# Kernel optimization log

Hardware: AMD Instinct MI355X
Metric: run time of the kernel (lower is better)

Reference implementation:

```python
import jax, jax.numpy as jnp
import numpy as np

N, E, D, NHID, NOUT, G = 100000, 600000, 128, 512, 768, 2048
EPS = 1e-5

def _lin_init(k, fi, fo):
    s = 1.0 / np.sqrt(fi)
    kw, kb = jax.random.split(k)
    W = jax.random.uniform(kw, (fi, fo), jnp.float32, -s, s)
    b = jax.random.uniform(kb, (fo,), jnp.float32, -s, s)
    return W, b

def setup_inputs():
    key = jax.random.key(0)
    ks = jax.random.split(key, 16)
    inp = {}
    inp['x'] = jax.random.normal(ks[0], (N, D), jnp.float32)
    inp['edge_index'] = jax.random.randint(ks[1], (2, E), 0, N, jnp.int32)
    inp['batch'] = jnp.sort(jax.random.randint(ks[2], (N,), 0, G, jnp.int32))
    # 3 GCN layers + GAT attention layer + 4 MLP linears
    inp['W1'], inp['b1'] = _lin_init(ks[3], D, D)
    inp['W2'], inp['b2'] = _lin_init(ks[4], D, D)
    inp['W3'], inp['b3'] = _lin_init(ks[5], D, D)
    inp['Wa'], inp['ba'] = _lin_init(ks[6], D, D)
    ka1, ka2 = jax.random.split(ks[7])
    inp['a_src'] = jax.random.normal(ka1, (D,), jnp.float32) * 0.1
    inp['a_dst'] = jax.random.normal(ka2, (D,), jnp.float32) * 0.1
    # batchnorm affine params (4 BNs)
    for i, nm in enumerate(['g1', 'g2', 'g3', 'ga']):
        inp[nm] = jnp.ones((D,), jnp.float32)
        inp['be' + nm[1:]] = jnp.zeros((D,), jnp.float32)
    inp['Wl1'], inp['bl1'] = _lin_init(ks[8], D, NHID)
    inp['Wl2'], inp['bl2'] = _lin_init(ks[9], NHID, NHID)
    inp['Wl3'], inp['bl3'] = _lin_init(ks[10], NHID, NHID)
    inp['Wl4'], inp['bl4'] = _lin_init(ks[11], NHID, NOUT)
    inp['gln'] = jnp.ones((NOUT,), jnp.float32)
    inp['bln'] = jnp.zeros((NOUT,), jnp.float32)
    return inp

def _bn(x, g, b):
    # training-mode batchnorm over node dim (biased variance, like torch)
    mu = jnp.mean(x, axis=0)
    var = jnp.var(x, axis=0)
    return (x - mu) * jax.lax.rsqrt(var + EPS) * g + b

def _forward(x, edge_index, batch, W1, b1, g1, be1, W2, b2, g2, be2, W3, b3, g3, be3,
             Wa, ba, a_src, a_dst, ga, bea, Wl1, bl1, Wl2, bl2, Wl3, bl3, Wl4, bl4, gln, bln):
    loop = jnp.arange(N, dtype=edge_index.dtype)
    src = jnp.concatenate([edge_index[0], loop])  # [E+N] with self-loops
    dst = jnp.concatenate([edge_index[1], loop])
    deg = jax.ops.segment_sum(jnp.ones_like(dst, jnp.float32), dst, num_segments=N)
    dinv = jax.lax.rsqrt(deg)  # deg >= 1 thanks to self-loops
    norm = (dinv[src] * dinv[dst])[:, None]  # [E+N, 1]

    def gcn(h, W, b):
        h = h @ W
        return jax.ops.segment_sum(h[src] * norm, dst, num_segments=N) + b

    x = jax.nn.relu(_bn(gcn(x, W1, b1), g1, be1)) + x
    x = jax.nn.relu(_bn(gcn(x, W2, b2), g2, be2)) + x
    x = jax.nn.relu(_bn(gcn(x, W3, b3), g3, be3)) + x

    # GATConv, heads=1: edge logit = LeakyReLU(a_src.h_j + a_dst.h_i), softmax over dst
    h = x @ Wa
    al = h @ a_src  # [N]
    ar = h @ a_dst
    e = jax.nn.leaky_relu(al[src] + ar[dst], 0.2)  # [E+N]
    m = jax.ops.segment_max(e, dst, num_segments=N)
    ee = jnp.exp(e - m[dst])
    denom = jax.ops.segment_sum(ee, dst, num_segments=N)
    alpha = (ee / denom[dst])[:, None]
    x = jax.ops.segment_sum(alpha * h[src], dst, num_segments=N) + ba
    x = jax.nn.relu(_bn(x, ga, bea))

    # global_add_pool
    x = jax.ops.segment_sum(x, batch, num_segments=G)  # [G, D]

    x = jax.nn.relu(x @ Wl1 + bl1)
    x = jax.nn.relu(x @ Wl2 + bl2)
    x = jax.nn.relu(x @ Wl3 + bl3)
    x = x @ Wl4 + bl4
    mu = jnp.mean(x, axis=-1, keepdims=True)
    var = jnp.var(x, axis=-1, keepdims=True)
    return (x - mu) * jax.lax.rsqrt(var + EPS) * gln + bln

def reference(x, edge_index, batch, W1, b1, g1, be1, W2, b2, g2, be2, W3, b3, g3, be3,
              Wa, ba, a_src, a_dst, ga, bea, Wl1, bl1, Wl2, bl2, Wl3, bl3, Wl4, bl4, gln, bln):
    return _forward(x, edge_index, batch, W1, b1, g1, be1, W2, b2, g2, be2, W3, b3, g3, be3,
                    Wa, ba, a_src, a_dst, ga, bea, Wl1, bl1, Wl2, bl2, Wl3, bl3, Wl4, bl4, gln, bln)
```

## Files before the change

kernel.cpp:

```cpp
#include <hip/hip_runtime.h>
#include <cstdint>
#include <cstddef>

#define CDIV(a,b) (((a)+(b)-1)/(b))

constexpr int N_ = 100000;
constexpr int E_ = 600000;
constexpr int D_ = 128;
constexpr int G_ = 2048;
constexpr int NHID_ = 512;
constexpr int NOUT_ = 768;
constexpr float EPS_ = 1e-5f;
constexpr int AGG_BLOCKS = 2048;

typedef short bf16x8 __attribute__((ext_vector_type(8)));
typedef float f32x4 __attribute__((ext_vector_type(4)));

__device__ __forceinline__ float wave_sum(float v){
#pragma unroll
  for (int m = 32; m; m >>= 1) v += __shfl_xor(v, m, 64);
  return v;
}
__device__ __forceinline__ float lrelu02(float v){ return v > 0.f ? v : 0.2f * v; }
__device__ __forceinline__ unsigned short f2bf(float f){
  unsigned u = __float_as_uint(f);
  u += 0x7FFF + ((u >> 16) & 1);
  return (unsigned short)(u >> 16);
}
__device__ __forceinline__ float bflo(unsigned u){ return __uint_as_float(u << 16); }
__device__ __forceinline__ float bfhi(unsigned u){ return __uint_as_float(u & 0xFFFF0000u); }

__device__ __forceinline__ float4 unplo(uint4 u){ return make_float4(bflo(u.x), bflo(u.y), bflo(u.z), bflo(u.w)); }
__device__ __forceinline__ float4 unphi(uint4 u){ return make_float4(bfhi(u.x), bfhi(u.y), bfhi(u.z), bfhi(u.w)); }
__device__ __forceinline__ float4 bnrelu4(float4 v, float4 sc, float4 sh){
  return make_float4(fmaxf(v.x*sc.x+sh.x, 0.f), fmaxf(v.y*sc.y+sh.y, 0.f),
                     fmaxf(v.z*sc.z+sh.z, 0.f), fmaxf(v.w*sc.w+sh.w, 0.f));
}
__device__ __forceinline__ float4 add4(float4 a, float4 b){
  return make_float4(a.x+b.x, a.y+b.y, a.z+b.z, a.w+b.w);
}
__device__ __forceinline__ uint4 pk4(float4 lo, float4 hi){
  uint4 u;
  u.x = (unsigned)f2bf(lo.x) | ((unsigned)f2bf(hi.x) << 16);
  u.y = (unsigned)f2bf(lo.y) | ((unsigned)f2bf(hi.y) << 16);
  u.z = (unsigned)f2bf(lo.z) | ((unsigned)f2bf(hi.z) << 16);
  u.w = (unsigned)f2bf(lo.w) | ((unsigned)f2bf(hi.w) << 16);
  return u;
}
__device__ __forceinline__ bf16x8 mkaf(float4 lo, float4 hi){
  bf16x8 a;
  a[0]=(short)f2bf(lo.x); a[1]=(short)f2bf(lo.y); a[2]=(short)f2bf(lo.z); a[3]=(short)f2bf(lo.w);
  a[4]=(short)f2bf(hi.x); a[5]=(short)f2bf(hi.y); a[6]=(short)f2bf(hi.z); a[7]=(short)f2bf(hi.w);
  return a;
}

__global__ void k_count(const int* __restrict__ dst, int* __restrict__ cnt){
  int e = blockIdx.x * 256 + threadIdx.x;
  if (e < E_) atomicAdd(&cnt[dst[e]], 1);
}

__global__ void k_dinv(const int* __restrict__ cnt, float* __restrict__ dinv){
  int i = blockIdx.x * 256 + threadIdx.x;
  if (i < N_) dinv[i] = rsqrtf((float)(cnt[i] + 1));
}

__global__ void k_scan1(const int* __restrict__ cnt, int* __restrict__ ro, int* __restrict__ bs){
  __shared__ int s[256];
  int tid = threadIdx.x;
  int i = blockIdx.x * 256 + tid;
  int v = (i < N_) ? cnt[i] : 0;
  s[tid] = v; __syncthreads();
  for (int off = 1; off < 256; off <<= 1){
    int add = (tid >= off) ? s[tid - off] : 0;
    __syncthreads();
    s[tid] += add;
    __syncthreads();
  }
  if (i < N_) ro[i] = s[tid] - v;
  if (tid == 255) bs[blockIdx.x] = s[255];
}

__global__ void k_scan2(int* __restrict__ bs, int nb){
  __shared__ int s[512];
  int t = threadIdx.x;
  int v = (t < nb) ? bs[t] : 0;
  s[t] = v; __syncthreads();
  for (int off = 1; off < 512; off <<= 1){
    int a = (t >= off) ? s[t - off] : 0;
    __syncthreads();
    s[t] += a;
    __syncthreads();
  }
  if (t < nb) bs[t] = s[t] - v;
}

__global__ void k_scan3(int* __restrict__ ro, const int* __restrict__ bs){
  int i = blockIdx.x * 256 + threadIdx.x;
  if (i < N_) ro[i] += bs[i >> 8];
  if (i == N_) ro[N_] = E_;
}

__global__ void k_fill(const int* __restrict__ src, const int* __restrict__ dst,
                       const int* __restrict__ ro, int* __restrict__ cur, int* __restrict__ csr){
  int e = blockIdx.x * 256 + threadIdx.x;
  if (e < E_){
    int d = dst[e];
    int p = atomicAdd(&cur[d], 1);
    csr[ro[d] + p] = src[e];
  }
}

__global__ void k_bounds(const int* __restrict__ batch, int* __restrict__ gs){
  int g = blockIdx.x * 256 + threadIdx.x;
  if (g > G_) return;
  int lo = 0, hi = N_;
  while (lo < hi){ int mid = (lo + hi) >> 1; if (batch[mid] < g) lo = mid + 1; else hi = mid; }
  gs[g] = lo;
}

__global__ void k_wprep(const float* __restrict__ W, short* __restrict__ Wt){
  int i = blockIdx.x * 256 + threadIdx.x;
  if (i >= 128 * 16) return;
  int c = i >> 4, tg = i & 15, t = tg >> 2, g = tg & 3;
  short* o = Wt + (size_t)i * 8;
#pragma unroll
  for (int j = 0; j < 8; ++j){
    int k = t * 32 + (j >> 2) * 16 + g * 4 + (j & 3);
    o[j] = (short)f2bf(W[(size_t)k * 128 + c]);
  }
}

template<bool XB, bool RB>
__global__ __launch_bounds__(256) void k_mm_mfma(const void* __restrict__ Xin,
                                                 const short* __restrict__ Wt,
                                                 unsigned* __restrict__ hout,
                                                 const float* __restrict__ ss,
                                                 const void* __restrict__ resin,
                                                 unsigned* __restrict__ xnew,
                                                 const float* __restrict__ prescale,
                                                 const float* __restrict__ asrc,
                                                 const float* __restrict__ adst,
                                                 float* __restrict__ al_out,
                                                 float* __restrict__ ar_out){
  int lane = threadIdx.x & 63, wid = threadIdx.x >> 6;
  int cl = lane & 15, g = lane >> 4;
  int r0a = blockIdx.x * 128 + wid * 16;
  int r0b = r0a + 64;
  int rowa = r0a + cl, rowb = r0b + cl;
  bool va_ = rowa < N_, vb_ = rowb < N_;
  int rma = va_ ? rowa : 0;
  int rmb = vb_ ? rowb : 0;

  uint4 xua[4], xub[4];
  float4 xfa[8], xfb[8];
  uint4 rua[4], rub[4];
  float4 rfa[8], rfb[8];
  bool has_res = resin != nullptr;
  if (XB){
    const uint4* Xa = (const uint4*)((const unsigned*)Xin + (size_t)rma * 64);
    const uint4* Xb = (const uint4*)((const unsigned*)Xin + (size_t)rmb * 64);
#pragma unroll
    for (int t = 0; t < 4; ++t){ xua[t] = Xa[t*4 + g]; xub[t] = Xb[t*4 + g]; }
  } else {
    const float4* Xa = (const float4*)((const float*)Xin + (size_t)rma * 128);
    const float4* Xb = (const float4*)((const float*)Xin + (size_t)rmb * 128);
#pragma unroll
    for (int t = 0; t < 4; ++t){
      xfa[2*t] = Xa[t*8 + g]; xfa[2*t+1] = Xa[t*8 + g + 4];
      xfb[2*t] = Xb[t*8 + g]; xfb[2*t+1] = Xb[t*8 + g + 4];
    }
  }
  if (has_res){
    if (RB){
      const uint4* Ra = (const uint4*)((const unsigned*)resin + (size_t)rma * 64);
      const uint4* Rb = (const uint4*)((const unsigned*)resin + (size_t)rmb * 64);
#pragma unroll
      for (int t = 0; t < 4; ++t){ rua[t] = Ra[t*4 + g]; rub[t] = Rb[t*4 + g]; }
    } else {
      const float4* Ra = (const float4*)((const float*)resin + (size_t)rma * 128);
      const float4* Rb = (const float4*)((const float*)resin + (size_t)rmb * 128);
#pragma unroll
      for (int t = 0; t < 4; ++t){
        rfa[2*t] = Ra[t*8 + g]; rfa[2*t+1] = Ra[t*8 + g + 4];
        rfb[2*t] = Rb[t*8 + g]; rfb[2*t+1] = Rb[t*8 + g + 4];
      }
    }
  }
  __builtin_amdgcn_sched_barrier(0);

  bf16x8 afa[4], afb[4];
#pragma unroll
  for (int t = 0; t < 4; ++t){
    float4 la, ha, lb, hb;
    if (XB){
      la = unplo(xua[t]); ha = unphi(xua[t]);
      lb = unplo(xub[t]); hb = unphi(xub[t]);
    } else {
      la = xfa[2*t]; ha = xfa[2*t+1];
      lb = xfb[2*t]; hb = xfb[2*t+1];
    }
    if (ss){
      int f0 = t * 32 + g * 4;
      float4 sc0 = *(const float4*)&ss[f0],      sh0 = *(const float4*)&ss[128 + f0];
      float4 sc1 = *(const float4*)&ss[f0 + 16], sh1 = *(const float4*)&ss[128 + f0 + 16];
      la = bnrelu4(la, sc0, sh0); ha = bnrelu4(ha, sc1, sh1);
      lb = bnrelu4(lb, sc0, sh0); hb = bnrelu4(hb, sc1, sh1);
      if (has_res){
        if (RB){
          la = add4(la, unplo(rua[t])); ha = add4(ha, unphi(rua[t]));
          lb = add4(lb, unplo(rub[t])); hb = add4(hb, unphi(rub[t]));
        } else {
          la = add4(la, rfa[2*t]); ha = add4(ha, rfa[2*t+1]);
          lb = add4(lb, rfb[2*t]); hb = add4(hb, rfb[2*t+1]);
        }
      }
      if (xnew){
        if (va_) *(uint4*)(xnew + (size_t)rowa * 64 + t*16 + g*4) = pk4(la, ha);
        if (vb_) *(uint4*)(xnew + (size_t)rowb * 64 + t*16 + g*4) = pk4(lb, hb);
      }
    }
    afa[t] = mkaf(la, ha);
    afb[t] = mkaf(lb, hb);
  }

  f32x4 accA[8], accB[8];
#pragma unroll
  for (int j = 0; j < 8; ++j){ accA[j] = (f32x4){0,0,0,0}; accB[j] = (f32x4){0,0,0,0}; }
#pragma unroll
  for (int t = 0; t < 4; ++t){
#pragma unroll
    for (int j = 0; j < 8; ++j){
      int c = j * 16 + cl;
      bf16x8 bf = *(const bf16x8*)(Wt + ((size_t)c * 16 + t * 4 + g) * 8);
      accA[j] = __builtin_amdgcn_mfma_f32_16x16x32_bf16(afa[t], bf, accA[j], 0, 0, 0);
      accB[j] = __builtin_amdgcn_mfma_f32_16x16x32_bf16(afb[t], bf, accB[j], 0, 0, 0);
    }
  }

#pragma unroll
  for (int r = 0; r < 4; ++r){
    int ra = r0a + g * 4 + r;
    if (ra < N_){
      float psc = prescale ? prescale[ra] : 1.f;
#pragma unroll
      for (int jp = 0; jp < 4; ++jp){
        unsigned lo = f2bf(accA[2*jp][r] * psc);
        unsigned hi = f2bf(accA[2*jp+1][r] * psc);
        hout[(size_t)ra * 64 + jp * 16 + cl] = (hi << 16) | lo;
      }
    }
    int rb = r0b + g * 4 + r;
    if (rb < N_){
      float psc = prescale ? prescale[rb] : 1.f;
#pragma unroll
      for (int jp = 0; jp < 4; ++jp){
        unsigned lo = f2bf(accB[2*jp][r] * psc);
        unsigned hi = f2bf(accB[2*jp+1][r] * psc);
        hout[(size_t)rb * 64 + jp * 16 + cl] = (hi << 16) | lo;
      }
    }
  }

  if (al_out){
    float pal[8] = {0,0,0,0,0,0,0,0}, par[8] = {0,0,0,0,0,0,0,0};
#pragma unroll
    for (int j = 0; j < 8; ++j){
      float as_ = asrc[j * 16 + cl], ad_ = adst[j * 16 + cl];
#pragma unroll
      for (int r = 0; r < 4; ++r){
        pal[r]   += accA[j][r] * as_; par[r]   += accA[j][r] * ad_;
        pal[4+r] += accB[j][r] * as_; par[4+r] += accB[j][r] * ad_;
      }
    }
#pragma unroll
    for (int m = 1; m < 16; m <<= 1)
#pragma unroll
      for (int r = 0; r < 8; ++r){
        pal[r] += __shfl_xor(pal[r], m, 64);
        par[r] += __shfl_xor(par[r], m, 64);
      }
    if (cl == 0){
#pragma unroll
      for (int r = 0; r < 4; ++r){
        int ra = r0a + g * 4 + r;
        if (ra < N_){ al_out[ra] = pal[r]; ar_out[ra] = par[r]; }
        int rb = r0b + g * 4 + r;
        if (rb < N_){ al_out[rb] = pal[4+r]; ar_out[rb] = par[4+r]; }
      }
    }
  }
}

__global__ __launch_bounds__(256) void k_gcn_agg2(const unsigned* __restrict__ hbf, const int* __restrict__ ro,
                          const int* __restrict__ csr, const float* __restrict__ dinv,
                          const float* __restrict__ bias, unsigned* __restrict__ outb,
                          float4* __restrict__ pbuf){
  int wid = threadIdx.x >> 6, lane = threadIdx.x & 63;
  int f0 = 32 * (lane >> 4) + (lane & 15), f1 = f0 + 16;
  float bb0 = bias[f0], bb1 = bias[f1];
  float S0 = 0.f, S1 = 0.f, Q0 = 0.f, Q1 = 0.f;
  for (int node = blockIdx.x * 4 + wid; node < N_; node += AGG_BLOCKS * 4){
    int s0 = ro[node], s1 = ro[node + 1];
    int deg = s1 - s0;
    float di = dinv[node];
    unsigned us = hbf[(size_t)node * 64 + lane];
    float a0 = bflo(us), a1 = bfhi(us);
    if (deg <= 64){
      int sidx = (lane < deg) ? csr[s0 + lane] : 0;
      int j = 0;
      for (; j + 4 <= deg; j += 4){
        int sa = __shfl(sidx, j, 64),   sb = __shfl(sidx, j+1, 64);
        int sc = __shfl(sidx, j+2, 64), sd = __shfl(sidx, j+3, 64);
        unsigned ua = hbf[(size_t)sa*64+lane], ub = hbf[(size_t)sb*64+lane];
        unsigned uc = hbf[(size_t)sc*64+lane], ud = hbf[(size_t)sd*64+lane];
        a0 += bflo(ua) + bflo(ub) + bflo(uc) + bflo(ud);
        a1 += bfhi(ua) + bfhi(ub) + bfhi(uc) + bfhi(ud);
      }
      for (; j < deg; ++j){
        int s = __shfl(sidx, j, 64);
        unsigned u = hbf[(size_t)s*64+lane];
        a0 += bflo(u); a1 += bfhi(u);
      }
    } else {
      for (int base = s0; base < s1; base += 64){
        int c = min(64, s1 - base);
        int sidx = (lane < c) ? csr[base + lane] : 0;
        for (int j = 0; j < c; ++j){
          int s = __shfl(sidx, j, 64);
          unsigned u = hbf[(size_t)s*64+lane];
          a0 += bflo(u); a1 += bfhi(u);
        }
      }
    }
    float o0 = di * a0 + bb0;
    float o1 = di * a1 + bb1;
    outb[(size_t)node * 64 + lane] = (unsigned)f2bf(o0) | ((unsigned)f2bf(o1) << 16);
    S0 += o0; S1 += o1; Q0 += o0*o0; Q1 += o1*o1;
  }
  __shared__ float4 sred[4][64];
  sred[wid][lane] = make_float4(S0, S1, Q0, Q1);
  __syncthreads();
  if (wid == 0){
    float4 t = sred[0][lane];
    float4 u1 = sred[1][lane], u2 = sred[2][lane], u3 = sred[3][lane];
    t.x += u1.x + u2.x + u3.x;
    t.y += u1.y + u2.y + u3.y;
    t.z += u1.z + u2.z + u3.z;
    t.w += u1.w + u2.w + u3.w;
    pbuf[(size_t)blockIdx.x * 64 + lane] = t;
  }
}

__global__ __launch_bounds__(256) void k_gat_agg2(const unsigned* __restrict__ hbf, const int* __restrict__ ro,
                          const int* __restrict__ csr, const float* __restrict__ al,
                          const float* __restrict__ ar, const float* __restrict__ bias,
                          unsigned* __restrict__ outb, float4* __restrict__ pbuf){
  int wid = threadIdx.x >> 6, lane = threadIdx.x & 63;
  int f0 = 32 * (lane >> 4) + (lane & 15), f1 = f0 + 16;
  float bb0 = bias[f0], bb1 = bias[f1];
  float S0 = 0.f, S1 = 0.f, Q0 = 0.f, Q1 = 0.f;
  for (int node = blockIdx.x * 4 + wid; node < N_; node += AGG_BLOCKS * 4){
    int s0 = ro[node], s1 = ro[node + 1];
    int deg = s1 - s0;
    float ari = ar[node], ali = al[node];
    float pself = __expf(lrelu02(ali + ari));
    unsigned uself = hbf[(size_t)node * 64 + lane];
    float h0 = bflo(uself), h1 = bfhi(uself);
    float a0, a1;
    if (deg <= 64){
      int sidx = 0; float p = 0.f;
      if (lane < deg){ sidx = csr[s0 + lane]; p = __expf(lrelu02(al[sidx] + ari)); }
      float invd = 1.f / (wave_sum(p) + pself);
      float wl = p * invd;
      float wsf = pself * invd;
      a0 = wsf * h0; a1 = wsf * h1;
      int j = 0;
      for (; j + 4 <= deg; j += 4){
        int sa = __shfl(sidx, j, 64),   sb = __shfl(sidx, j+1, 64);
        int sc = __shfl(sidx, j+2, 64), sd = __shfl(sidx, j+3, 64);
        float wa = __shfl(wl, j, 64),   wb = __shfl(wl, j+1, 64);
        float wc = __shfl(wl, j+2, 64), wd = __shfl(wl, j+3, 64);
        unsigned ua = hbf[(size_t)sa*64+lane], ub = hbf[(size_t)sb*64+lane];
        unsigned uc = hbf[(size_t)sc*64+lane], ud = hbf[(size_t)sd*64+lane];
        a0 += wa*bflo(ua) + wb*bflo(ub) + wc*bflo(uc) + wd*bflo(ud);
        a1 += wa*bfhi(ua) + wb*bfhi(ub) + wc*bfhi(uc) + wd*bfhi(ud);
      }
      for (; j < deg; ++j){
        int s = __shfl(sidx, j, 64); float w = __shfl(wl, j, 64);
        unsigned u = hbf[(size_t)s*64+lane];
        a0 += w*bflo(u); a1 += w*bfhi(u);
      }
    } else {
      float denom = pself;
      for (int base = s0; base < s1; base += 64){
        int c = min(64, s1 - base);
        float p = 0.f;
        if (lane < c) p = __expf(lrelu02(al[csr[base + lane]] + ari));
        denom += wave_sum(p);
      }
      float invd = 1.f / denom;
      float wsf = pself * invd;
      a0 = wsf * h0; a1 = wsf * h1;
      for (int base = s0; base < s1; base += 64){
        int c = min(64, s1 - base);
        int sidx = 0; float wl = 0.f;
        if (lane < c){ sidx = csr[base + lane]; wl = __expf(lrelu02(al[sidx] + ari)) * invd; }
        for (int j = 0; j < c; ++j){
          int s = __shfl(sidx, j, 64); float w = __shfl(wl, j, 64);
          unsigned u = hbf[(size_t)s*64+lane];
          a0 += w*bflo(u); a1 += w*bfhi(u);
        }
      }
    }
    float o0 = a0 + bb0, o1 = a1 + bb1;
    outb[(size_t)node * 64 + lane] = (unsigned)f2bf(o0) | ((unsigned)f2bf(o1) << 16);
    S0 += o0; S1 += o1; Q0 += o0*o0; Q1 += o1*o1;
  }
  __shared__ float4 sred[4][64];
  sred[wid][lane] = make_float4(S0, S1, Q0, Q1);
  __syncthreads();
  if (wid == 0){
    float4 t = sred[0][lane];
    float4 u1 = sred[1][lane], u2 = sred[2][lane], u3 = sred[3][lane];
    t.x += u1.x + u2.x + u3.x;
    t.y += u1.y + u2.y + u3.y;
    t.z += u1.z + u2.z + u3.z;
    t.w += u1.w + u2.w + u3.w;
    pbuf[(size_t)blockIdx.x * 64 + lane] = t;
  }
}

__global__ void k_bn_reduce(const float4* __restrict__ pbuf, const float* __restrict__ g,
                            const float* __restrict__ be, float* __restrict__ ss){
  int c = blockIdx.x;
  int f0 = 32 * (c >> 4) + (c & 15), f1 = f0 + 16;
  float4 a = make_float4(0.f, 0.f, 0.f, 0.f);
  for (int r = threadIdx.x; r < AGG_BLOCKS; r += 256){
    float4 v = pbuf[(size_t)r * 64 + c];
    a.x += v.x; a.y += v.y; a.z += v.z; a.w += v.w;
  }
  __shared__ float4 s[256];
  s[threadIdx.x] = a; __syncthreads();
  for (int off = 128; off; off >>= 1){
    if (threadIdx.x < off){
      float4 o = s[threadIdx.x + off];
      s[threadIdx.x].x += o.x; s[threadIdx.x].y += o.y;
      s[threadIdx.x].z += o.z; s[threadIdx.x].w += o.w;
    }
    __syncthreads();
  }
  if (threadIdx.x == 0){
    float4 t = s[0];
    float inv_n = 1.f / (float)N_;
    float mean0 = t.x * inv_n, mean1 = t.y * inv_n;
    float var0 = fmaxf(t.z * inv_n - mean0 * mean0, 0.f);
    float var1 = fmaxf(t.w * inv_n - mean1 * mean1, 0.f);
    float sc0 = g[f0] * rsqrtf(var0 + EPS_);
    float sc1 = g[f1] * rsqrtf(var1 + EPS_);
    ss[f0] = sc0; ss[f1] = sc1;
    ss[128 + f0] = be[f0] - mean0 * sc0;
    ss[128 + f1] = be[f1] - mean1 * sc1;
  }
}

__global__ void k_pool2(const unsigned* __restrict__ xn, const int* __restrict__ gs,
                        const float* __restrict__ ss, float* __restrict__ pooled){
  int g = blockIdx.x, f = threadIdx.x & 127, half = threadIdx.x >> 7;
  int idx = ((f >> 5) << 4) | (f & 15);
  int hi = (f >> 4) & 1;
  int s = gs[g], e = gs[g + 1];
  float sc = ss[f], sh = ss[128 + f];
  float a = 0.f;
  for (int n = s + half; n < e; n += 2){
    unsigned u = xn[(size_t)n * 64 + idx];
    float v = hi ? bfhi(u) : bflo(u);
    a += fmaxf(v * sc + sh, 0.f);
  }
  __shared__ float red[256];
  red[threadIdx.x] = a; __syncthreads();
  if (half == 0) pooled[(size_t)g * 128 + f] = red[threadIdx.x] + red[threadIdx.x + 128];
}

__global__ __launch_bounds__(256) void k_gemm(const float* __restrict__ A, const float* __restrict__ W,
                                              const float* __restrict__ bias, float* __restrict__ C,
                                              int M, int K, int Nc, int relu){
  __shared__ float As[64][17];
  __shared__ float Ws[16][64];
  int tid = threadIdx.x;
  int ty = tid >> 4, tx = tid & 15;
  int rb = blockIdx.y * 64, cb = blockIdx.x * 64;
  float acc[4][4] = {};
  for (int k0 = 0; k0 < K; k0 += 16){
    {
      int r = tid >> 2, kq = tid & 3;
      float4 v = *(const float4*)&A[(size_t)(rb + r) * K + k0 + kq * 4];
      As[r][kq*4+0] = v.x; As[r][kq*4+1] = v.y; As[r][kq*4+2] = v.z; As[r][kq*4+3] = v.w;
    }
    {
      int kk = tid >> 4, cq = tid & 15;
      float4 v = *(const float4*)&W[(size_t)(k0 + kk) * Nc + cb + cq * 4];
      *(float4*)&Ws[kk][cq * 4] = v;
    }
    __syncthreads();
#pragma unroll
    for (int k = 0; k < 16; ++k){
      float a0 = As[ty*4+0][k], a1 = As[ty*4+1][k], a2 = As[ty*4+2][k], a3 = As[ty*4+3][k];
      float b0 = Ws[k][tx], b1 = Ws[k][tx+16], b2 = Ws[k][tx+32], b3 = Ws[k][tx+48];
      acc[0][0] += a0*b0; acc[0][1] += a0*b1; acc[0][2] += a0*b2; acc[0][3] += a0*b3;
      acc[1][0] += a1*b0; acc[1][1] += a1*b1; acc[1][2] += a1*b2; acc[1][3] += a1*b3;
      acc[2][0] += a2*b0; acc[2][1] += a2*b1; acc[2][2] += a2*b2; acc[2][3] += a2*b3;
      acc[3][0] += a3*b0; acc[3][1] += a3*b1; acc[3][2] += a3*b2; acc[3][3] += a3*b3;
    }
    __syncthreads();
  }
#pragma unroll
  for (int i = 0; i < 4; ++i)
#pragma unroll
    for (int j = 0; j < 4; ++j){
      int c = cb + tx + 16 * j;
      float v = acc[i][j] + bias[c];
      if (relu) v = fmaxf(v, 0.f);
      C[(size_t)(rb + ty*4 + i) * Nc + c] = v;
    }
}

__global__ void k_layernorm(const float* __restrict__ xin, const float* __restrict__ g,
                            const float* __restrict__ b, float* __restrict__ out){
  __shared__ float red[8];
  int row = blockIdx.x, tid = threadIdx.x;
  float v0 = xin[(size_t)row*768 + tid];
  float v1 = xin[(size_t)row*768 + tid + 256];
  float v2 = xin[(size_t)row*768 + tid + 512];
  float s = v0 + v1 + v2;
  float q = v0*v0 + v1*v1 + v2*v2;
  s = wave_sum(s); q = wave_sum(q);
  int wid = tid >> 6;
  if ((tid & 63) == 0){ red[wid] = s; red[4 + wid] = q; }
  __syncthreads();
  if (tid == 0){
    float ts = red[0] + red[1] + red[2] + red[3];
    float tq = red[4] + red[5] + red[6] + red[7];
    float mean = ts / 768.f;
    float var = tq / 768.f - mean * mean;
    red[0] = mean; red[1] = rsqrtf(fmaxf(var, 0.f) + EPS_);
  }
  __syncthreads();
  float mean = red[0], inv = red[1];
  out[(size_t)row*768 + tid]       = (v0 - mean) * inv * g[tid]       + b[tid];
  out[(size_t)row*768 + tid + 256] = (v1 - mean) * inv * g[tid + 256] + b[tid + 256];
  out[(size_t)row*768 + tid + 512] = (v2 - mean) * inv * g[tid + 512] + b[tid + 512];
}

extern "C" void kernel_launch(void* const* d_in, const int* in_sizes, int n_in,
                              void* d_out, int out_size, void* d_ws, size_t ws_size,
                              hipStream_t stream){
  const float* x     = (const float*)d_in[0];
  const int*   ei    = (const int*)d_in[1];
  const int*   src   = ei;
  const int*   dst   = ei + E_;
  const int*   batch = (const int*)d_in[2];
  const float* W1 = (const float*)d_in[3];  const float* b1 = (const float*)d_in[4];
  const float* W2 = (const float*)d_in[5];  const float* b2 = (const float*)d_in[6];
  const float* W3 = (const float*)d_in[7];  const float* b3 = (const float*)d_in[8];
  const float* Wa = (const float*)d_in[9];  const float* ba = (const float*)d_in[10];
  const float* a_src = (const float*)d_in[11]; const float* a_dst = (const float*)d_in[12];
  const float* g1 = (const float*)d_in[13]; const float* be1 = (const float*)d_in[14];
  const float* g2 = (const float*)d_in[15]; const float* be2 = (const float*)d_in[16];
  const float* g3 = (const float*)d_in[17]; const float* be3 = (const float*)d_in[18];
  const float* ga = (const float*)d_in[19]; const float* bea = (const float*)d_in[20];
  const float* Wl1 = (const float*)d_in[21]; const float* bl1 = (const float*)d_in[22];
  const float* Wl2 = (const float*)d_in[23]; const float* bl2 = (const float*)d_in[24];
  const float* Wl3 = (const float*)d_in[25]; const float* bl3 = (const float*)d_in[26];
  const float* Wl4 = (const float*)d_in[27]; const float* bl4 = (const float*)d_in[28];
  const float* gln = (const float*)d_in[29]; const float* bln = (const float*)d_in[30];
  float* out = (float*)d_out;

  char* base = (char*)d_ws;
  size_t off = 0;
  auto alloc = [&](size_t bytes)->char*{
    char* p = base + off;
    off += (bytes + 255) & ~(size_t)255;
    return p;
  };
  int*   cnt    = (int*)  alloc((size_t)N_ * 4);
  float* dinv   = (float*)alloc((size_t)N_ * 4);
  int*   ro     = (int*)  alloc((size_t)(N_ + 1) * 4);
  int*   bs     = (int*)  alloc(512 * 4);
  int*   cur    = (int*)  alloc((size_t)N_ * 4);
  int*   csr    = (int*)  alloc((size_t)E_ * 4);
  int*   gstart = (int*)  alloc((size_t)(G_ + 1) * 4);
  float* al     = (float*)alloc((size_t)N_ * 4);
  float* ar     = (float*)alloc((size_t)N_ * 4);
  float* ss     = (float*)alloc(256 * 4);
  float4* pbuf  = (float4*)alloc((size_t)AGG_BLOCKS * 64 * 16);
  short* wt1    = (short*)alloc((size_t)128 * 128 * 2);
  short* wt2    = (short*)alloc((size_t)128 * 128 * 2);
  short* wt3    = (short*)alloc((size_t)128 * 128 * 2);
  short* wta    = (short*)alloc((size_t)128 * 128 * 2);
  unsigned* bufH  = (unsigned*)alloc((size_t)N_ * 64 * 4);
  unsigned* bufYb = (unsigned*)alloc((size_t)N_ * 64 * 4);
  unsigned* xresb = (unsigned*)alloc((size_t)N_ * 64 * 4);
  float* pooled = (float*)alloc((size_t)G_ * D_ * 4);
  float* m1     = (float*)alloc((size_t)G_ * NHID_ * 4);
  float* m2     = (float*)alloc((size_t)G_ * NHID_ * 4);
  float* m4     = (float*)alloc((size_t)G_ * NOUT_ * 4);
  (void)ws_size; (void)in_sizes; (void)n_in; (void)out_size;

  const int nbE = CDIV(E_, 256), nbN = CDIV(N_, 256);
  const int MMB = CDIV(N_, 128);

  hipMemsetAsync(cnt, 0, (size_t)N_ * 4, stream);
  k_count<<<nbE, 256, 0, stream>>>(dst, cnt);
  k_dinv<<<nbN, 256, 0, stream>>>(cnt, dinv);
  k_scan1<<<nbN, 256, 0, stream>>>(cnt, ro, bs);
  k_scan2<<<1, 512, 0, stream>>>(bs, nbN);
  k_scan3<<<CDIV(N_ + 1, 256), 256, 0, stream>>>(ro, bs);
  hipMemsetAsync(cur, 0, (size_t)N_ * 4, stream);
  k_fill<<<nbE, 256, 0, stream>>>(src, dst, ro, cur, csr);
  k_bounds<<<CDIV(G_ + 1, 256), 256, 0, stream>>>(batch, gstart);
  k_wprep<<<8, 256, 0, stream>>>(W1, wt1);
  k_wprep<<<8, 256, 0, stream>>>(W2, wt2);
  k_wprep<<<8, 256, 0, stream>>>(W3, wt3);
  k_wprep<<<8, 256, 0, stream>>>(Wa, wta);

  k_mm_mfma<false,false><<<MMB, 256, 0, stream>>>(x, wt1, bufH, nullptr, nullptr, nullptr,
                                                  dinv, nullptr, nullptr, nullptr, nullptr);
  k_gcn_agg2<<<AGG_BLOCKS, 256, 0, stream>>>(bufH, ro, csr, dinv, b1, bufYb, pbuf);
  k_bn_reduce<<<64, 256, 0, stream>>>(pbuf, g1, be1, ss);
  k_mm_mfma<true,false><<<MMB, 256, 0, stream>>>(bufYb, wt2, bufH, ss, x, xresb,
                                                 dinv, nullptr, nullptr, nullptr, nullptr);
  k_gcn_agg2<<<AGG_BLOCKS, 256, 0, stream>>>(bufH, ro, csr, dinv, b2, bufYb, pbuf);
  k_bn_reduce<<<64, 256, 0, stream>>>(pbuf, g2, be2, ss);
  k_mm_mfma<true,true><<<MMB, 256, 0, stream>>>(bufYb, wt3, bufH, ss, xresb, xresb,
                                                dinv, nullptr, nullptr, nullptr, nullptr);
  k_gcn_agg2<<<AGG_BLOCKS, 256, 0, stream>>>(bufH, ro, csr, dinv, b3, bufYb, pbuf);
  k_bn_reduce<<<64, 256, 0, stream>>>(pbuf, g3, be3, ss);
  k_mm_mfma<true,true><<<MMB, 256, 0, stream>>>(bufYb, wta, bufH, ss, xresb, nullptr,
                                                nullptr, a_src, a_dst, al, ar);
  k_gat_agg2<<<AGG_BLOCKS, 256, 0, stream>>>(bufH, ro, csr, al, ar, ba, bufYb, pbuf);
  k_bn_reduce<<<64, 256, 0, stream>>>(pbuf, ga, bea, ss);
  k_pool2<<<G_, 256, 0, stream>>>(bufYb, gstart, ss, pooled);
  k_gemm<<<dim3(NHID_/64, G_/64), 256, 0, stream>>>(pooled, Wl1, bl1, m1, G_, D_, NHID_, 1);
  k_gemm<<<dim3(NHID_/64, G_/64), 256, 0, stream>>>(m1, Wl2, bl2, m2, G_, NHID_, NHID_, 1);
  k_gemm<<<dim3(NHID_/64, G_/64), 256, 0, stream>>>(m2, Wl3, bl3, m1, G_, NHID_, NHID_, 1);
  k_gemm<<<dim3(NOUT_/64, G_/64), 256, 0, stream>>>(m1, Wl4, bl4, m4, G_, NHID_, NOUT_, 0);
  k_layernorm<<<G_, 256, 0, stream>>>(m4, gln, bln, out);
}
```

Before: 556.8 us.

## Replace FP32 MLP GEMMs with bf16 MFMA GEMMs and bf16 intermediates

The four post-pooling MLP linears move from a scalar FP32 shared-memory GEMM to a bf16 MFMA kernel that reads prepacked transposed weights. The pooled features and hidden activations are now stored as packed bf16, which halves their memory traffic. The weight prep kernel is generalized to any K and N, adding four more prep launches. The cost is bf16 precision in the MLP chain, and the new GEMM loads weights straight from global memory with no LDS reuse.

```diff
diff --git a/kernel.cpp b/kernel.cpp
--- a/kernel.cpp
+++ b/kernel.cpp
@@ -51,6 +51,14 @@
   bf16x8 a;
   a[0]=(short)f2bf(lo.x); a[1]=(short)f2bf(lo.y); a[2]=(short)f2bf(lo.z); a[3]=(short)f2bf(lo.w);
   a[4]=(short)f2bf(hi.x); a[5]=(short)f2bf(hi.y); a[6]=(short)f2bf(hi.z); a[7]=(short)f2bf(hi.w);
+  return a;
+}
+__device__ __forceinline__ bf16x8 mkaf_u(uint4 u){
+  bf16x8 a;
+  a[0]=(short)(u.x & 0xFFFF); a[4]=(short)(u.x >> 16);
+  a[1]=(short)(u.y & 0xFFFF); a[5]=(short)(u.y >> 16);
+  a[2]=(short)(u.z & 0xFFFF); a[6]=(short)(u.z >> 16);
+  a[3]=(short)(u.w & 0xFFFF); a[7]=(short)(u.w >> 16);
   return a;
 }
 
@@ -118,15 +126,17 @@
   gs[g] = lo;
 }
 
-__global__ void k_wprep(const float* __restrict__ W, short* __restrict__ Wt){
+__global__ void k_wprep_g(const float* __restrict__ W, short* __restrict__ Wt, int K, int N){
   int i = blockIdx.x * 256 + threadIdx.x;
-  if (i >= 128 * 16) return;
-  int c = i >> 4, tg = i & 15, t = tg >> 2, g = tg & 3;
+  int KT = K >> 5;
+  int total = N * KT * 4;
+  if (i >= total) return;
+  int g = i & 3, t = (i >> 2) % KT, c = i / (KT * 4);
   short* o = Wt + (size_t)i * 8;
 #pragma unroll
   for (int j = 0; j < 8; ++j){
     int k = t * 32 + (j >> 2) * 16 + g * 4 + (j & 3);
-    o[j] = (short)f2bf(W[(size_t)k * 128 + c]);
+    o[j] = (short)f2bf(W[(size_t)k * N + c]);
   }
 }
 
@@ -464,7 +474,7 @@
 }
 
 __global__ void k_pool2(const unsigned* __restrict__ xn, const int* __restrict__ gs,
-                        const float* __restrict__ ss, float* __restrict__ pooled){
+                        const float* __restrict__ ss, unsigned* __restrict__ pooled){
   int g = blockIdx.x, f = threadIdx.x & 127, half = threadIdx.x >> 7;
   int idx = ((f >> 5) << 4) | (f & 15);
   int hi = (f >> 4) & 1;
@@ -478,50 +488,69 @@
   }
   __shared__ float red[256];
   red[threadIdx.x] = a; __syncthreads();
-  if (half == 0) pooled[(size_t)g * 128 + f] = red[threadIdx.x] + red[threadIdx.x + 128];
-}
-
-__global__ __launch_bounds__(256) void k_gemm(const float* __restrict__ A, const float* __restrict__ W,
-                                              const float* __restrict__ bias, float* __restrict__ C,
-                                              int M, int K, int Nc, int relu){
-  __shared__ float As[64][17];
-  __shared__ float Ws[16][64];
-  int tid = threadIdx.x;
-  int ty = tid >> 4, tx = tid & 15;
-  int rb = blockIdx.y * 64, cb = blockIdx.x * 64;
-  float acc[4][4] = {};
-  for (int k0 = 0; k0 < K; k0 += 16){
-    {
-      int r = tid >> 2, kq = tid & 3;
-      float4 v = *(const float4*)&A[(size_t)(rb + r) * K + k0 + kq * 4];
-      As[r][kq*4+0] = v.x; As[r][kq*4+1] = v.y; As[r][kq*4+2] = v.z; As[r][kq*4+3] = v.w;
-    }
-    {
-      int kk = tid >> 4, cq = tid & 15;
-      float4 v = *(const float4*)&W[(size_t)(k0 + kk) * Nc + cb + cq * 4];
-      *(float4*)&Ws[kk][cq * 4] = v;
-    }
-    __syncthreads();
-#pragma unroll
-    for (int k = 0; k < 16; ++k){
-      float a0 = As[ty*4+0][k], a1 = As[ty*4+1][k], a2 = As[ty*4+2][k], a3 = As[ty*4+3][k];
-      float b0 = Ws[k][tx], b1 = Ws[k][tx+16], b2 = Ws[k][tx+32], b3 = Ws[k][tx+48];
-      acc[0][0] += a0*b0; acc[0][1] += a0*b1; acc[0][2] += a0*b2; acc[0][3] += a0*b3;
-      acc[1][0] += a1*b0; acc[1][1] += a1*b1; acc[1][2] += a1*b2; acc[1][3] += a1*b3;
-      acc[2][0] += a2*b0; acc[2][1] += a2*b1; acc[2][2] += a2*b2; acc[2][3] += a2*b3;
-      acc[3][0] += a3*b0; acc[3][1] += a3*b1; acc[3][2] += a3*b2; acc[3][3] += a3*b3;
-    }
-    __syncthreads();
-  }
-#pragma unroll
-  for (int i = 0; i < 4; ++i)
-#pragma unroll
-    for (int j = 0; j < 4; ++j){
-      int c = cb + tx + 16 * j;
-      float v = acc[i][j] + bias[c];
-      if (relu) v = fmaxf(v, 0.f);
-      C[(size_t)(rb + ty*4 + i) * Nc + c] = v;
-    }
+  if (half == 0 && hi == 0){
+    float vlo = red[f] + red[f + 128];
+    float vhi = red[f + 16] + red[f + 16 + 128];
+    pooled[(size_t)g * 64 + idx] = (unsigned)f2bf(vlo) | ((unsigned)f2bf(vhi) << 16);
+  }
+}
+
+template<int K, bool RELU, bool OUTF32>
+__global__ __launch_bounds__(256) void k_gemm_mfma(const unsigned* __restrict__ A,
+                                                   const short* __restrict__ Wt,
+                                                   const float* __restrict__ bias,
+                                                   void* __restrict__ Cout, int Ncols){
+  constexpr int KT = K >> 5;
+  int lane = threadIdx.x & 63, wid = threadIdx.x >> 6;
+  int cl = lane & 15, g = lane >> 4;
+  int row0 = blockIdx.y * 64 + wid * 16;
+  int cb = blockIdx.x;
+  int arow = row0 + cl;
+  const uint4* Ar = (const uint4*)(A + (size_t)arow * (K / 2));
+
+  f32x4 acc[8];
+#pragma unroll
+  for (int j = 0; j < 8; ++j) acc[j] = (f32x4){0,0,0,0};
+
+  for (int t = 0; t < KT; ++t){
+    bf16x8 af = mkaf_u(Ar[t*4 + g]);
+#pragma unroll
+    for (int j = 0; j < 8; ++j){
+      int c = cb * 128 + j * 16 + cl;
+      bf16x8 bf = *(const bf16x8*)(Wt + (((size_t)c * KT + t) * 4 + g) * 8);
+      acc[j] = __builtin_amdgcn_mfma_f32_16x16x32_bf16(af, bf, acc[j], 0, 0, 0);
+    }
+  }
+
+  if (OUTF32){
+    float* C = (float*)Cout;
+#pragma unroll
+    for (int r = 0; r < 4; ++r){
+      int row = row0 + g * 4 + r;
+#pragma unroll
+      for (int j = 0; j < 8; ++j){
+        int c = cb * 128 + j * 16 + cl;
+        float v = acc[j][r] + bias[c];
+        if (RELU) v = fmaxf(v, 0.f);
+        C[(size_t)row * Ncols + c] = v;
+      }
+    }
+  } else {
+    unsigned* C = (unsigned*)Cout;
+#pragma unroll
+    for (int r = 0; r < 4; ++r){
+      int row = row0 + g * 4 + r;
+#pragma unroll
+      for (int jp = 0; jp < 4; ++jp){
+        int clo = cb * 128 + jp * 32 + cl;
+        float vlo = acc[2*jp][r] + bias[clo];
+        float vhi = acc[2*jp+1][r] + bias[clo + 16];
+        if (RELU){ vlo = fmaxf(vlo, 0.f); vhi = fmaxf(vhi, 0.f); }
+        C[(size_t)row * (Ncols / 2) + (cb * 4 + jp) * 16 + cl] =
+            (unsigned)f2bf(vlo) | ((unsigned)f2bf(vhi) << 16);
+      }
+    }
+  }
 }
 
 __global__ void k_layernorm(const float* __restrict__ xin, const float* __restrict__ g,
@@ -597,12 +626,16 @@
   short* wt2    = (short*)alloc((size_t)128 * 128 * 2);
   short* wt3    = (short*)alloc((size_t)128 * 128 * 2);
   short* wta    = (short*)alloc((size_t)128 * 128 * 2);
+  short* wtl1   = (short*)alloc((size_t)128 * NHID_ * 2);
+  short* wtl2   = (short*)alloc((size_t)NHID_ * NHID_ * 2);
+  short* wtl3   = (short*)alloc((size_t)NHID_ * NHID_ * 2);
+  short* wtl4   = (short*)alloc((size_t)NHID_ * NOUT_ * 2);
   unsigned* bufH  = (unsigned*)alloc((size_t)N_ * 64 * 4);
   unsigned* bufYb = (unsigned*)alloc((size_t)N_ * 64 * 4);
   unsigned* xresb = (unsigned*)alloc((size_t)N_ * 64 * 4);
-  float* pooled = (float*)alloc((size_t)G_ * D_ * 4);
-  float* m1     = (float*)alloc((size_t)G_ * NHID_ * 4);
-  float* m2     = (float*)alloc((size_t)G_ * NHID_ * 4);
+  unsigned* pooled= (unsigned*)alloc((size_t)G_ * 64 * 4);
+  unsigned* m1b   = (unsigned*)alloc((size_t)G_ * (NHID_/2) * 4);
+  unsigned* m2b   = (unsigned*)alloc((size_t)G_ * (NHID_/2) * 4);
   float* m4     = (float*)alloc((size_t)G_ * NOUT_ * 4);
   (void)ws_size; (void)in_sizes; (void)n_in; (void)out_size;
 
@@ -618,10 +651,14 @@
   hipMemsetAsync(cur, 0, (size_t)N_ * 4, stream);
   k_fill<<<nbE, 256, 0, stream>>>(src, dst, ro, cur, csr);
   k_bounds<<<CDIV(G_ + 1, 256), 256, 0, stream>>>(batch, gstart);
-  k_wprep<<<8, 256, 0, stream>>>(W1, wt1);
-  k_wprep<<<8, 256, 0, stream>>>(W2, wt2);
-  k_wprep<<<8, 256, 0, stream>>>(W3, wt3);
-  k_wprep<<<8, 256, 0, stream>>>(Wa, wta);
+  k_wprep_g<<<8, 256, 0, stream>>>(W1, wt1, 128, 128);
+  k_wprep_g<<<8, 256, 0, stream>>>(W2, wt2, 128, 128);
+  k_wprep_g<<<8, 256, 0, stream>>>(W3, wt3, 128, 128);
+  k_wprep_g<<<8, 256, 0, stream>>>(Wa, wta, 128, 128);
+  k_wprep_g<<<CDIV(NHID_*4*4, 256), 256, 0, stream>>>(Wl1, wtl1, 128, NHID_);
+  k_wprep_g<<<CDIV(NHID_*16*4, 256), 256, 0, stream>>>(Wl2, wtl2, NHID_, NHID_);
+  k_wprep_g<<<CDIV(NHID_*16*4, 256), 256, 0, stream>>>(Wl3, wtl3, NHID_, NHID_);
+  k_wprep_g<<<CDIV(NOUT_*16*4, 256), 256, 0, stream>>>(Wl4, wtl4, NHID_, NOUT_);
 
   k_mm_mfma<false,false><<<MMB, 256, 0, stream>>>(x, wt1, bufH, nullptr, nullptr, nullptr,
                                                   dinv, nullptr, nullptr, nullptr, nullptr);
@@ -640,9 +677,9 @@
   k_gat_agg2<<<AGG_BLOCKS, 256, 0, stream>>>(bufH, ro, csr, al, ar, ba, bufYb, pbuf);
   k_bn_reduce<<<64, 256, 0, stream>>>(pbuf, ga, bea, ss);
   k_pool2<<<G_, 256, 0, stream>>>(bufYb, gstart, ss, pooled);
-  k_gemm<<<dim3(NHID_/64, G_/64), 256, 0, stream>>>(pooled, Wl1, bl1, m1, G_, D_, NHID_, 1);
-  k_gemm<<<dim3(NHID_/64, G_/64), 256, 0, stream>>>(m1, Wl2, bl2, m2, G_, NHID_, NHID_, 1);
-  k_gemm<<<dim3(NHID_/64, G_/64), 256, 0, stream>>>(m2, Wl3, bl3, m1, G_, NHID_, NHID_, 1);
-  k_gemm<<<dim3(NOUT_/64, G_/64), 256, 0, stream>>>(m1, Wl4, bl4, m4, G_, NHID_, NOUT_, 0);
+  k_gemm_mfma<128, true, false><<<dim3(NHID_/128, G_/64), 256, 0, stream>>>(pooled, wtl1, bl1, m1b, NHID_);
+  k_gemm_mfma<512, true, false><<<dim3(NHID_/128, G_/64), 256, 0, stream>>>(m1b, wtl2, bl2, m2b, NHID_);
+  k_gemm_mfma<512, true, false><<<dim3(NHID_/128, G_/64), 256, 0, stream>>>(m2b, wtl3, bl3, m1b, NHID_);
+  k_gemm_mfma<512, false, true><<<dim3(NOUT_/128, G_/64), 256, 0, stream>>>(m1b, wtl4, bl4, m4, NOUT_);
   k_layernorm<<<G_, 256, 0, stream>>>(m4, gln, bln, out);
 }
```

Result: no change. 550.6 us (-1.1%).
